# Optimization experiments

Hardware: AMD Instinct MI355X
Metric: run time of the kernel (lower is better)

Reference implementation:

```python
import jax, jax.numpy as jnp
import numpy as np

B, N, CIN, H, OUT, L, K = 8, 512, 64, 64, 64, 256, 3
EPS = 1e-5


def setup_inputs() -> dict:
    key = jax.random.key(0)
    ks = jax.random.split(key, 12)
    def unif(k, shape, fan):
        s = 1.0 / np.sqrt(fan)
        return jax.random.uniform(k, shape, jnp.float32, -s, s)
    return {
        "x": jax.random.normal(ks[0], (B, N, CIN, L), jnp.float32),
        "adj": jax.random.uniform(ks[1], (B, N, N), jnp.float32),
        # temp_conv1: Conv1d(CIN->H, k=3)
        "w1": unif(ks[2], (H, CIN, K), CIN * K),
        "b1": unif(ks[3], (H,), CIN * K),
        # graph_conv: Linear-style (H,H) + bias, stdv=1/sqrt(out_features)
        "gw": unif(ks[4], (H, H), H),
        "gb": unif(ks[5], (H,), H),
        # temp_conv2: Conv1d(H->OUT, k=3)
        "w2": unif(ks[6], (OUT, H, K), H * K),
        "b2": unif(ks[7], (OUT,), H * K),
        # residual: Conv1d(CIN->OUT, k=1) == pointwise linear
        "wr": unif(ks[8], (OUT, CIN), CIN),
        "br": unif(ks[9], (OUT,), CIN),
        # BatchNorm2d(OUT) affine params
        "gamma": jnp.ones((OUT,), jnp.float32),
        "beta": jnp.zeros((OUT,), jnp.float32),
    }


def _conv1d(x, w, b, pad):
    # x: (B, N, C, L) -> flatten node dim into batch, NCH conv
    b_, n_, c, l = x.shape
    y = jax.lax.conv_general_dilated(
        x.reshape(b_ * n_, c, l), w, window_strides=(1,),
        padding=[(pad, pad)], dimension_numbers=("NCH", "OIH", "NCH"))
    y = y + b[None, :, None]
    return y.reshape(b_, n_, w.shape[0], l)


def reference(x, adj, w1, b1, gw, gb, w2, b2, wr, br, gamma, beta):
    pad = (K - 1) // 2
    # residual branch: 1x1 conv over channels
    residual = jnp.einsum("bncl,oc->bnol", x, wr) + br[None, None, :, None]
    # temporal conv 1
    out = _conv1d(x, w1, b1, pad)                      # (B,N,H,L)
    # graph conv over all timesteps at once (replaces per-t Python loop)
    xw = jnp.einsum("bnhl,hd->bndl", out, gw)          # (B,N,H,L)
    out = jnp.einsum("bnm,bmdl->bndl", adj, xw) + gb[None, None, :, None]
    # temporal conv 2
    out = _conv1d(out, w2, b2, pad)                    # (B,N,OUT,L)
    out = out + residual
    # BatchNorm2d over channel axis (training-mode batch stats, biased var)
    mean = jnp.mean(out, axis=(0, 1, 3), keepdims=True)
    var = jnp.mean(jnp.square(out - mean), axis=(0, 1, 3), keepdims=True)
    out = (out - mean) * jax.lax.rsqrt(var + EPS)
    out = out * gamma[None, None, :, None] + beta[None, None, :, None]
    return jax.nn.relu(out)
```

## Files before the change

### kernel.cpp

```cpp
#include <hip/hip_runtime.h>
#include <hip/hip_bf16.h>
#include <stdint.h>


typedef unsigned short u16;
typedef unsigned int   u32;
typedef __attribute__((ext_vector_type(8))) short           bf16x8;
typedef __attribute__((ext_vector_type(8))) unsigned short  u16x8;
typedef __attribute__((ext_vector_type(4))) unsigned short  u16x4;
typedef __attribute__((ext_vector_type(4))) float           f32x4;

__device__ __forceinline__ float bf2f(u16 v){
  union { u32 u; float f; } x; x.u = ((u32)v) << 16; return x.f;
}
__device__ __forceinline__ u16 f2bf(float f){
  __hip_bfloat16 h = __float2bfloat16(f);
  return *reinterpret_cast<u16*>(&h);
}
__device__ __forceinline__ u32 swz(int row, int cbyte){
  return (u32)(row * 128) + (u32)(cbyte ^ ((row & 7) << 4));
}

__device__ __forceinline__ void stage_Tf(const float* __restrict__ src, u16* dst, int t){
  const int c0 = (t & 31) * 2;
  const int l0 = (t >> 5) * 32;
  #pragma unroll
  for (int v = 0; v < 8; ++v){
    f32x4 a = *(const f32x4*)(src + (size_t)c0 * 256 + l0 + v * 4);
    f32x4 b = *(const f32x4*)(src + (size_t)(c0 + 1) * 256 + l0 + v * 4);
    #pragma unroll
    for (int e = 0; e < 4; ++e){
      u32 p = (u32)f2bf(a[e]) | ((u32)f2bf(b[e]) << 16);
      *(u32*)((char*)dst + swz(l0 + v * 4 + e, c0 * 2)) = p;
    }
  }
}
__device__ __forceinline__ void stage_Tb(const u16* __restrict__ src, u16* dst, int t){
  const int c0 = (t & 31) * 2;
  const int l0 = (t >> 5) * 32;
  #pragma unroll
  for (int v = 0; v < 4; ++v){
    u16x8 a = *(const u16x8*)(src + (size_t)c0 * 256 + l0 + v * 8);
    u16x8 b = *(const u16x8*)(src + (size_t)(c0 + 1) * 256 + l0 + v * 8);
    #pragma unroll
    for (int e = 0; e < 8; ++e){
      u32 p = (u32)a[e] | ((u32)b[e] << 16);
      *(u32*)((char*)dst + swz(l0 + v * 8 + e, c0 * 2)) = p;
    }
  }
}

__global__ __launch_bounds__(256) void k_prep(const float* __restrict__ w1, const float* __restrict__ b1,
    const float* __restrict__ gw, const float* __restrict__ w2, const float* __restrict__ wr,
    u16* __restrict__ w1g, float* __restrict__ b1g, u16* __restrict__ w2t, u16* __restrict__ wrt){
  const int gt = blockIdx.x * 256 + threadIdx.x, gs = gridDim.x * 256;
  for (int e = gt; e < 12288; e += gs){
    int tap = e >> 12, rem = e & 4095, o = rem >> 6, c = rem & 63;
    w2t[e] = f2bf(w2[(o * 64 + c) * 3 + tap]);
    float s = 0.f;
    for (int h = 0; h < 64; ++h)
      s += gw[h * 64 + o] * w1[(h * 64 + c) * 3 + tap];
    w1g[e] = f2bf(s);
  }
  for (int e = gt; e < 4096; e += gs) wrt[e] = f2bf(wr[e]);
  for (int d = gt; d < 64; d += gs){
    float s = 0.f;
    for (int h = 0; h < 64; ++h) s += b1[h] * gw[h * 64 + d];
    b1g[d] = s;
  }
}

__global__ __launch_bounds__(256) void k_p1(const float* __restrict__ x,
    const u16* __restrict__ w1g, const float* __restrict__ b1g,
    const u16* __restrict__ wrt, u16* __restrict__ outA, u16* __restrict__ outR){
  __shared__ u16 tile[16384];
  const int t = threadIdx.x;
  const size_t bn = (size_t)blockIdx.x + (size_t)blockIdx.y * 512;
  stage_Tf(x + bn * 16384, tile, t);
  __syncthreads();
  const int w = t >> 6, ln = t & 63, lq = ln >> 4, lr = ln & 15;
  const bf16x8 z8 = {};

  {
    f32x4 racc[4][4];
    #pragma unroll
    for (int i = 0; i < 4; ++i)
      #pragma unroll
      for (int j = 0; j < 4; ++j) racc[i][j] = (f32x4){0.f, 0.f, 0.f, 0.f};
    #pragma unroll
    for (int kk = 0; kk < 2; ++kk){
      bf16x8 A[4];
      #pragma unroll
      for (int fo = 0; fo < 4; ++fo)
        A[fo] = *(const bf16x8*)(wrt + (fo * 16 + lr) * 64 + kk * 32 + lq * 8);
      #pragma unroll
      for (int fc = 0; fc < 4; ++fc){
        int l = w * 64 + fc * 16 + lr;
        bf16x8 B = *(const bf16x8*)((char*)tile + swz(l, kk * 64 + lq * 16));
        #pragma unroll
        for (int fo = 0; fo < 4; ++fo)
          racc[fo][fc] = __builtin_amdgcn_mfma_f32_16x16x32_bf16(A[fo], B, racc[fo][fc], 0, 0, 0);
      }
    }
    u16* rp = outR + bn * 16384 + t * 64;
    #pragma unroll
    for (int v = 0; v < 8; ++v){
      u16x8 ov;
      const int fo = v >> 1;
      #pragma unroll
      for (int h = 0; h < 2; ++h){
        const int fc = (v & 1) * 2 + h;
        #pragma unroll
        for (int r2 = 0; r2 < 4; ++r2)
          ov[h * 4 + r2] = f2bf(racc[fo][fc][r2]);
      }
      *(u16x8*)(rp + v * 8) = ov;
    }
  }

  f32x4 acc[4][4];
  #pragma unroll
  for (int i = 0; i < 4; ++i)
    #pragma unroll
    for (int j = 0; j < 4; ++j) acc[i][j] = (f32x4){0.f, 0.f, 0.f, 0.f};
  #pragma unroll
  for (int tap = 0; tap < 3; ++tap){
    #pragma unroll
    for (int kk = 0; kk < 2; ++kk){
      bf16x8 A[4];
      #pragma unroll
      for (int fo = 0; fo < 4; ++fo)
        A[fo] = *(const bf16x8*)(w1g + tap * 4096 + (fo * 16 + lr) * 64 + kk * 32 + lq * 8);
      #pragma unroll
      for (int fc = 0; fc < 4; ++fc){
        int r = w * 64 + fc * 16 + lr + tap - 1;
        int rc = r < 0 ? 0 : (r > 255 ? 255 : r);
        bf16x8 B = *(const bf16x8*)((char*)tile + swz(rc, kk * 64 + lq * 16));
        if (r != rc) B = z8;
        #pragma unroll
        for (int fo = 0; fo < 4; ++fo)
          acc[fo][fc] = __builtin_amdgcn_mfma_f32_16x16x32_bf16(A[fo], B, acc[fo][fc], 0, 0, 0);
      }
    }
  }
  u16* op = outA + bn * 16384;
  #pragma unroll
  for (int fo = 0; fo < 4; ++fo){
    float bb[4];
    #pragma unroll
    for (int r2 = 0; r2 < 4; ++r2) bb[r2] = b1g[fo * 16 + lq * 4 + r2];
    #pragma unroll
    for (int fc = 0; fc < 4; ++fc){
      int l = w * 64 + fc * 16 + lr;
      #pragma unroll
      for (int r2 = 0; r2 < 4; ++r2)
        op[(fo * 16 + lq * 4 + r2) * 256 + l] = f2bf(acc[fo][fc][r2] + bb[r2]);
    }
  }
}

__global__ __launch_bounds__(256) void k_p3(const u16* __restrict__ xw,
    const float* __restrict__ adj, const float* __restrict__ gbv, u16* __restrict__ outB){
  __shared__ u16 At[8192];
  __shared__ u16 Bt[8192];
  const int t = threadIdx.x;
  const int wg = ((blockIdx.x & 7) << 9) | ((int)blockIdx.x >> 3);
  const int jt = wg & 127, nt = (wg >> 7) & 3, b = wg >> 9;
  const float* adjb = adj + ((size_t)b * 512 + (size_t)nt * 128) * 512;
  const u16* Xb = xw + (size_t)b * 8388608 + (size_t)jt * 128;
  const int w = t >> 6, ln = t & 63, lq = ln >> 4, lr = ln & 15;
  const int wrow = w >> 1, wcol = w & 1;
  const int mpair = t & 31, jq = t >> 5;
  f32x4 acc[4][4];
  #pragma unroll
  for (int i = 0; i < 4; ++i)
    #pragma unroll
    for (int j = 0; j < 4; ++j) acc[i][j] = (f32x4){0.f, 0.f, 0.f, 0.f};

  f32x4 ra[8];
  u16x8 rb[4];
  auto LOADK = [&](int ks){
    #pragma unroll
    for (int it = 0; it < 8; ++it){
      int c = it * 256 + t;
      int row = c >> 4, mc = c & 15;
      ra[it] = *(const f32x4*)(adjb + (size_t)row * 512 + ks * 64 + mc * 4);
    }
    const u16* s0 = Xb + (size_t)(ks * 64 + mpair * 2) * 16384 + jq * 16;
    const u16* s1 = s0 + 16384;
    #pragma unroll
    for (int v2 = 0; v2 < 2; ++v2){
      rb[v2 * 2]     = *(const u16x8*)(s0 + v2 * 8);
      rb[v2 * 2 + 1] = *(const u16x8*)(s1 + v2 * 8);
    }
  };

  LOADK(0);
  for (int ks = 0; ks < 8; ++ks){
    #pragma unroll
    for (int it = 0; it < 8; ++it){
      int c = it * 256 + t;
      int row = c >> 4, mc = c & 15;
      u16x4 pk;
      #pragma unroll
      for (int e = 0; e < 4; ++e) pk[e] = f2bf(ra[it][e]);
      *(u16x4*)((char*)At + (u32)(row * 128) + (u32)((mc * 8) ^ ((row & 7) << 4))) = pk;
    }
    #pragma unroll
    for (int v2 = 0; v2 < 2; ++v2){
      #pragma unroll
      for (int e = 0; e < 8; ++e){
        u32 p = (u32)(u16)rb[v2 * 2][e] | ((u32)(u16)rb[v2 * 2 + 1][e] << 16);
        *(u32*)((char*)Bt + swz(jq * 16 + v2 * 8 + e, mpair * 4)) = p;
      }
    }
    __syncthreads();
    if (ks < 7) LOADK(ks + 1);
    #pragma unroll
    for (int kk = 0; kk < 2; ++kk){
      bf16x8 Af[4], Bf[4];
      #pragma unroll
      for (int f = 0; f < 4; ++f){
        int rA = wrow * 64 + f * 16 + lr;
        Af[f] = *(const bf16x8*)((char*)At + swz(rA, kk * 64 + lq * 16));
        int rB = wcol * 64 + f * 16 + lr;
        Bf[f] = *(const bf16x8*)((char*)Bt + swz(rB, kk * 64 + lq * 16));
      }
      #pragma unroll
      for (int fr = 0; fr < 4; ++fr)
        #pragma unroll
        for (int fc = 0; fc < 4; ++fc)
          acc[fr][fc] = __builtin_amdgcn_mfma_f32_16x16x32_bf16(Af[fr], Bf[fc], acc[fr][fc], 0, 0, 0);
    }
    __syncthreads();
  }
  const float gb = gbv[jt >> 1];
  u16* ob = outB + ((size_t)b * 512 + (size_t)nt * 128) * 16384 + (size_t)jt * 128;
  #pragma unroll
  for (int fr = 0; fr < 4; ++fr)
    #pragma unroll
    for (int fc = 0; fc < 4; ++fc)
      #pragma unroll
      for (int r2 = 0; r2 < 4; ++r2){
        int n_ = wrow * 64 + fr * 16 + lq * 4 + r2;
        int j_ = wcol * 64 + fc * 16 + lr;
        ob[(size_t)n_ * 16384 + j_] = f2bf(acc[fr][fc][r2] + gb);
      }
}

__global__ __launch_bounds__(256) void k_p4(const u16* __restrict__ g,
    const u16* __restrict__ resv, const u16* __restrict__ w2t,
    const float* __restrict__ b2v, const float* __restrict__ brv,
    u16* __restrict__ outP, float* __restrict__ spart){
  __shared__ u16 gt[16384];
  const int t = threadIdx.x;
  const size_t bn = (size_t)blockIdx.x + (size_t)blockIdx.y * 512;
  stage_Tb(g + bn * 16384, gt, t);
  __syncthreads();
  const int w = t >> 6, ln = t & 63, lq = ln >> 4, lr = ln & 15;
  const bf16x8 z8 = {};
  f32x4 acc[4][4];
  #pragma unroll
  for (int i = 0; i < 4; ++i)
    #pragma unroll
    for (int j = 0; j < 4; ++j) acc[i][j] = (f32x4){0.f, 0.f, 0.f, 0.f};

  #pragma unroll
  for (int tap = 0; tap < 3; ++tap){
    #pragma unroll
    for (int kk = 0; kk < 2; ++kk){
      bf16x8 A[4];
      #pragma unroll
      for (int fo = 0; fo < 4; ++fo)
        A[fo] = *(const bf16x8*)(w2t + tap * 4096 + (fo * 16 + lr) * 64 + kk * 32 + lq * 8);
      #pragma unroll
      for (int fc = 0; fc < 4; ++fc){
        int r = w * 64 + fc * 16 + lr + tap - 1;
        int rc = r < 0 ? 0 : (r > 255 ? 255 : r);
        bf16x8 B = *(const bf16x8*)((char*)gt + swz(rc, kk * 64 + lq * 16));
        if (r != rc) B = z8;
        #pragma unroll
        for (int fo = 0; fo < 4; ++fo)
          acc[fo][fc] = __builtin_amdgcn_mfma_f32_16x16x32_bf16(A[fo], B, acc[fo][fc], 0, 0, 0);
      }
    }
  }

  float bball[16];
  #pragma unroll
  for (int fo = 0; fo < 4; ++fo)
    #pragma unroll
    for (int r2 = 0; r2 < 4; ++r2){
      int o = fo * 16 + lq * 4 + r2;
      bball[fo * 4 + r2] = b2v[o] + brv[o];
    }
  float psum[16], psq[16];
  #pragma unroll
  for (int i = 0; i < 16; ++i){ psum[i] = 0.f; psq[i] = 0.f; }

  const u16* rp = resv + bn * 16384 + t * 64;
  u16x8 rv[8];
  #pragma unroll
  for (int v = 0; v < 8; ++v) rv[v] = *(const u16x8*)(rp + v * 8);

  u16* op = outP + bn * 16384;
  #pragma unroll
  for (int fo = 0; fo < 4; ++fo){
    #pragma unroll
    for (int fc = 0; fc < 4; ++fc){
      int l = w * 64 + fc * 16 + lr;
      #pragma unroll
      for (int r2 = 0; r2 < 4; ++r2){
        float val = acc[fo][fc][r2] + bball[fo * 4 + r2]
                  + bf2f(rv[fo * 2 + (fc >> 1)][(fc & 1) * 4 + r2]);
        op[(fo * 16 + lq * 4 + r2) * 256 + l] = f2bf(val);
        psum[fo * 4 + r2] += val;
        psq[fo * 4 + r2] += val * val;
      }
    }
  }

  #pragma unroll
  for (int i = 0; i < 16; ++i){
    #pragma unroll
    for (int m = 1; m < 16; m <<= 1){
      psum[i] += __shfl_xor(psum[i], m, 64);
      psq[i]  += __shfl_xor(psq[i],  m, 64);
    }
  }
  __syncthreads();
  float* sc = (float*)gt;
  if (lr == 0){
    #pragma unroll
    for (int i = 0; i < 16; ++i){
      int o = (i >> 2) * 16 + lq * 4 + (i & 3);
      sc[w * 128 + o]      = psum[i];
      sc[w * 128 + 64 + o] = psq[i];
    }
  }
  __syncthreads();
  if (t < 128){
    float tot = sc[t] + sc[128 + t] + sc[256 + t] + sc[384 + t];
    spart[(size_t)t * 4096 + bn] = tot;
  }
}

__global__ __launch_bounds__(256) void k_p5(const float* __restrict__ part, float* __restrict__ fin){
  const int o = blockIdx.x, t = threadIdx.x;
  float s1 = 0.f, s2 = 0.f;
  for (int k = t; k < 4096; k += 256){
    s1 += part[(size_t)o * 4096 + k];
    s2 += part[(size_t)(64 + o) * 4096 + k];
  }
  #pragma unroll
  for (int m = 32; m; m >>= 1){
    s1 += __shfl_down(s1, m, 64);
    s2 += __shfl_down(s2, m, 64);
  }
  __shared__ float red[8];
  if ((t & 63) == 0){ red[(t >> 6) * 2] = s1; red[(t >> 6) * 2 + 1] = s2; }
  __syncthreads();
  if (t == 0){
    float S1 = red[0] + red[2] + red[4] + red[6];
    float S2 = red[1] + red[3] + red[5] + red[7];
    const float invN = 1.f / 1048576.f;
    float mean = S1 * invN;
    float var = S2 * invN - mean * mean;
    fin[o] = mean;
    fin[64 + o] = rsqrtf(var + 1e-5f);
  }
}

__global__ __launch_bounds__(256) void k_p6(const u16* __restrict__ pre, const float* __restrict__ fin,
    const float* __restrict__ gamma, const float* __restrict__ beta, float* __restrict__ out){
  __shared__ float ssca[64], soff[64];
  const int tt = threadIdx.x;
  if (tt < 64){
    float sc = fin[64 + tt] * gamma[tt];
    ssca[tt] = sc;
    soff[tt] = beta[tt] - fin[tt] * sc;
  }
  __syncthreads();
  const size_t nchunk = 8388608;
  for (size_t i = (size_t)blockIdx.x * 256 + tt; i < nchunk; i += (size_t)gridDim.x * 256){
    int o = (int)((i >> 5) & 63);
    float sca = ssca[o], off = soff[o];
    u16x8 v = *(const u16x8*)(pre + i * 8);
    f32x4 oa, ob;
    #pragma unroll
    for (int e = 0; e < 4; ++e){
      float f0 = bf2f(v[e]) * sca + off;
      float f1 = bf2f(v[4 + e]) * sca + off;
      oa[e] = f0 > 0.f ? f0 : 0.f;
      ob[e] = f1 > 0.f ? f1 : 0.f;
    }
    *(f32x4*)(out + i * 8)     = oa;
    *(f32x4*)(out + i * 8 + 4) = ob;
  }
}

extern "C" void kernel_launch(void* const* d_in, const int* in_sizes, int n_in,
                              void* d_out, int out_size, void* d_ws, size_t ws_size,
                              hipStream_t stream){
  const float* x     = (const float*)d_in[0];
  const float* adj   = (const float*)d_in[1];
  const float* w1    = (const float*)d_in[2];
  const float* b1    = (const float*)d_in[3];
  const float* gw    = (const float*)d_in[4];
  const float* gb    = (const float*)d_in[5];
  const float* w2    = (const float*)d_in[6];
  const float* b2    = (const float*)d_in[7];
  const float* wr    = (const float*)d_in[8];
  const float* br    = (const float*)d_in[9];
  const float* gamma = (const float*)d_in[10];
  const float* beta  = (const float*)d_in[11];
  (void)in_sizes; (void)n_in; (void)out_size; (void)ws_size;

  char* ws = (char*)d_ws;
  u16*   bufA  = (u16*)ws;
  float* spart = (float*)(ws + 134217728);
  float* sfin  = (float*)(ws + 136314880);
  u16*   w1g   = (u16*)(ws + 136315392);
  float* b1g   = (float*)(ws + 136339968);
  u16*   w2t   = (u16*)(ws + 136348160);
  u16*   wrt   = (u16*)(ws + 136372736);
  u16*   gbuf  = (u16*)d_out;
  u16*   bufR  = (u16*)d_out + 67108864;

  k_prep<<<16, 256, 0, stream>>>(w1, b1, gw, w2, wr, w1g, b1g, w2t, wrt);
  k_p1<<<dim3(512, 8, 1), 256, 0, stream>>>(x, w1g, b1g, wrt, bufA, bufR);
  k_p3<<<4096, 256, 0, stream>>>(bufA, adj, gb, gbuf);
  k_p4<<<dim3(512, 8, 1), 256, 0, stream>>>(gbuf, bufR, w2t, b2, br, bufA, spart);
  k_p5<<<64, 256, 0, stream>>>(spart, sfin);
  k_p6<<<2048, 256, 0, stream>>>(bufA, sfin, gamma, beta, (float*)d_out);
}
```

Before: 573.1 us.

## Drop block barriers after LDS staging by making conv reads wave-local

In the first and second temporal-conv kernels, the __syncthreads after staging the input tile into LDS is removed. Each wave now clamps its LDS reads to the 64 rows it staged itself. The halo rows just outside that range are read directly from global memory, converting to bf16 in the first kernel, with zero padding kept at the sequence ends. The residual loads in the second kernel are also issued before the MMA loop so their latency overlaps compute. This removes block-wide synchronisation but adds strided scalar global loads for boundary lanes, and it is correct only if the staging routine assigns each wave exactly its own rows.

Measured after the change: 603.2 us. 1.05x slower.

```diff
diff --git a/kernel.cpp b/kernel.cpp
--- a/kernel.cpp
+++ b/kernel.cpp
@@ -76,9 +76,10 @@
   __shared__ u16 tile[16384];
   const int t = threadIdx.x;
   const size_t bn = (size_t)blockIdx.x + (size_t)blockIdx.y * 512;
-  stage_Tf(x + bn * 16384, tile, t);
-  __syncthreads();
+  const float* xb = x + bn * 16384;
+  stage_Tf(xb, tile, t);
   const int w = t >> 6, ln = t & 63, lq = ln >> 4, lr = ln & 15;
+  const int lo = w * 64, hi = w * 64 + 63;
   const bf16x8 z8 = {};
 
   {
@@ -127,6 +128,7 @@
   for (int tap = 0; tap < 3; ++tap){
     #pragma unroll
     for (int kk = 0; kk < 2; ++kk){
+      const int ch0 = kk * 32 + lq * 8;
       bf16x8 A[4];
       #pragma unroll
       for (int fo = 0; fo < 4; ++fo)
@@ -134,9 +136,18 @@
       #pragma unroll
       for (int fc = 0; fc < 4; ++fc){
         int r = w * 64 + fc * 16 + lr + tap - 1;
-        int rc = r < 0 ? 0 : (r > 255 ? 255 : r);
+        int rc = r < lo ? lo : (r > hi ? hi : r);
         bf16x8 B = *(const bf16x8*)((char*)tile + swz(rc, kk * 64 + lq * 16));
-        if (r != rc) B = z8;
+        if (r != rc){
+          if (r < 0 || r > 255) B = z8;
+          else {
+            bf16x8 f;
+            #pragma unroll
+            for (int e = 0; e < 8; ++e)
+              f[e] = (short)f2bf(xb[(ch0 + e) * 256 + r]);
+            B = f;
+          }
+        }
         #pragma unroll
         for (int fo = 0; fo < 4; ++fo)
           acc[fo][fc] = __builtin_amdgcn_mfma_f32_16x16x32_bf16(A[fo], B, acc[fo][fc], 0, 0, 0);
@@ -255,10 +266,17 @@
   __shared__ u16 gt[16384];
   const int t = threadIdx.x;
   const size_t bn = (size_t)blockIdx.x + (size_t)blockIdx.y * 512;
-  stage_Tb(g + bn * 16384, gt, t);
-  __syncthreads();
+  const u16* gb = g + bn * 16384;
+  stage_Tb(gb, gt, t);
   const int w = t >> 6, ln = t & 63, lq = ln >> 4, lr = ln & 15;
+  const int lo = w * 64, hi = w * 64 + 63;
   const bf16x8 z8 = {};
+
+  const u16* rp = resv + bn * 16384 + t * 64;
+  u16x8 rv[8];
+  #pragma unroll
+  for (int v = 0; v < 8; ++v) rv[v] = *(const u16x8*)(rp + v * 8);
+
   f32x4 acc[4][4];
   #pragma unroll
   for (int i = 0; i < 4; ++i)
@@ -269,6 +287,7 @@
   for (int tap = 0; tap < 3; ++tap){
     #pragma unroll
     for (int kk = 0; kk < 2; ++kk){
+      const int ch0 = kk * 32 + lq * 8;
       bf16x8 A[4];
       #pragma unroll
       for (int fo = 0; fo < 4; ++fo)
@@ -276,9 +295,18 @@
       #pragma unroll
       for (int fc = 0; fc < 4; ++fc){
         int r = w * 64 + fc * 16 + lr + tap - 1;
-        int rc = r < 0 ? 0 : (r > 255 ? 255 : r);
+        int rc = r < lo ? lo : (r > hi ? hi : r);
         bf16x8 B = *(const bf16x8*)((char*)gt + swz(rc, kk * 64 + lq * 16));
-        if (r != rc) B = z8;
+        if (r != rc){
+          if (r < 0 || r > 255) B = z8;
+          else {
+            bf16x8 f;
+            #pragma unroll
+            for (int e = 0; e < 8; ++e)
+              f[e] = (short)gb[(ch0 + e) * 256 + r];
+            B = f;
+          }
+        }
         #pragma unroll
         for (int fo = 0; fo < 4; ++fo)
           acc[fo][fc] = __builtin_amdgcn_mfma_f32_16x16x32_bf16(A[fo], B, acc[fo][fc], 0, 0, 0);
@@ -297,11 +325,6 @@
   float psum[16], psq[16];
   #pragma unroll
   for (int i = 0; i < 16; ++i){ psum[i] = 0.f; psq[i] = 0.f; }
-
-  const u16* rp = resv + bn * 16384 + t * 64;
-  u16x8 rv[8];
-  #pragma unroll
-  for (int v = 0; v < 8; ++v) rv[v] = *(const u16x8*)(rp + v * 8);
 
   u16* op = outP + bn * 16384;
   #pragma unroll
```

## Split output channels into two halves in conv kernels to raise occupancy

Applied to the files above, without the earlier changes.

In k_p1 and k_p4, each wave now computes its output channels in two passes of 32 channels, which halves the live accumulator arrays. The kernels gain launch bounds requesting four blocks per SM, and sched_barrier calls stop the compiler from merging the two passes. k_p4 writes its statistics to a separate shared buffer, removing one __syncthreads that previously guarded reuse of the tile. The cost is that B fragments are reloaded from LDS for each half, and the residual loads and shuffle reductions are split per half.

Measured after the change: 584.2 us. No clear change (+1.9%).

```diff
diff --git a/kernel.cpp b/kernel.cpp
--- a/kernel.cpp
+++ b/kernel.cpp
@@ -70,92 +70,99 @@
   }
 }
 
-__global__ __launch_bounds__(256) void k_p1(const float* __restrict__ x,
+__global__ __launch_bounds__(256, 4) void k_p1(const float* __restrict__ x,
     const u16* __restrict__ w1g, const float* __restrict__ b1g,
     const u16* __restrict__ wrt, u16* __restrict__ outA, u16* __restrict__ outR){
   __shared__ u16 tile[16384];
   const int t = threadIdx.x;
   const size_t bn = (size_t)blockIdx.x + (size_t)blockIdx.y * 512;
-  stage_Tf(x + bn * 16384, tile, t);
+  const float* xb = x + bn * 16384;
+  stage_Tf(xb, tile, t);
   __syncthreads();
   const int w = t >> 6, ln = t & 63, lq = ln >> 4, lr = ln & 15;
   const bf16x8 z8 = {};
 
-  {
-    f32x4 racc[4][4];
-    #pragma unroll
-    for (int i = 0; i < 4; ++i)
+  #pragma unroll
+  for (int h0 = 0; h0 < 2; ++h0){
+    f32x4 racc[2][4];
+    #pragma unroll
+    for (int i = 0; i < 2; ++i)
       #pragma unroll
       for (int j = 0; j < 4; ++j) racc[i][j] = (f32x4){0.f, 0.f, 0.f, 0.f};
     #pragma unroll
     for (int kk = 0; kk < 2; ++kk){
-      bf16x8 A[4];
-      #pragma unroll
-      for (int fo = 0; fo < 4; ++fo)
-        A[fo] = *(const bf16x8*)(wrt + (fo * 16 + lr) * 64 + kk * 32 + lq * 8);
+      bf16x8 A[2];
+      #pragma unroll
+      for (int fi = 0; fi < 2; ++fi)
+        A[fi] = *(const bf16x8*)(wrt + ((h0 * 2 + fi) * 16 + lr) * 64 + kk * 32 + lq * 8);
       #pragma unroll
       for (int fc = 0; fc < 4; ++fc){
         int l = w * 64 + fc * 16 + lr;
         bf16x8 B = *(const bf16x8*)((char*)tile + swz(l, kk * 64 + lq * 16));
         #pragma unroll
-        for (int fo = 0; fo < 4; ++fo)
-          racc[fo][fc] = __builtin_amdgcn_mfma_f32_16x16x32_bf16(A[fo], B, racc[fo][fc], 0, 0, 0);
-      }
-    }
-    u16* rp = outR + bn * 16384 + t * 64;
-    #pragma unroll
-    for (int v = 0; v < 8; ++v){
+        for (int fi = 0; fi < 2; ++fi)
+          racc[fi][fc] = __builtin_amdgcn_mfma_f32_16x16x32_bf16(A[fi], B, racc[fi][fc], 0, 0, 0);
+      }
+    }
+    u16* rp = outR + bn * 16384 + t * 64 + h0 * 32;
+    #pragma unroll
+    for (int v2 = 0; v2 < 4; ++v2){
       u16x8 ov;
-      const int fo = v >> 1;
-      #pragma unroll
-      for (int h = 0; h < 2; ++h){
-        const int fc = (v & 1) * 2 + h;
+      const int fi = v2 >> 1;
+      #pragma unroll
+      for (int hh = 0; hh < 2; ++hh){
+        const int fc = (v2 & 1) * 2 + hh;
         #pragma unroll
         for (int r2 = 0; r2 < 4; ++r2)
-          ov[h * 4 + r2] = f2bf(racc[fo][fc][r2]);
-      }
-      *(u16x8*)(rp + v * 8) = ov;
-    }
-  }
-
-  f32x4 acc[4][4];
-  #pragma unroll
-  for (int i = 0; i < 4; ++i)
-    #pragma unroll
-    for (int j = 0; j < 4; ++j) acc[i][j] = (f32x4){0.f, 0.f, 0.f, 0.f};
-  #pragma unroll
-  for (int tap = 0; tap < 3; ++tap){
-    #pragma unroll
-    for (int kk = 0; kk < 2; ++kk){
-      bf16x8 A[4];
-      #pragma unroll
-      for (int fo = 0; fo < 4; ++fo)
-        A[fo] = *(const bf16x8*)(w1g + tap * 4096 + (fo * 16 + lr) * 64 + kk * 32 + lq * 8);
+          ov[hh * 4 + r2] = f2bf(racc[fi][fc][r2]);
+      }
+      *(u16x8*)(rp + v2 * 8) = ov;
+    }
+    __builtin_amdgcn_sched_barrier(0);
+  }
+
+  u16* op = outA + bn * 16384;
+  #pragma unroll
+  for (int h0 = 0; h0 < 2; ++h0){
+    f32x4 acc[2][4];
+    #pragma unroll
+    for (int i = 0; i < 2; ++i)
+      #pragma unroll
+      for (int j = 0; j < 4; ++j) acc[i][j] = (f32x4){0.f, 0.f, 0.f, 0.f};
+    #pragma unroll
+    for (int tap = 0; tap < 3; ++tap){
+      #pragma unroll
+      for (int kk = 0; kk < 2; ++kk){
+        bf16x8 A[2];
+        #pragma unroll
+        for (int fi = 0; fi < 2; ++fi)
+          A[fi] = *(const bf16x8*)(w1g + tap * 4096 + ((h0 * 2 + fi) * 16 + lr) * 64 + kk * 32 + lq * 8);
+        #pragma unroll
+        for (int fc = 0; fc < 4; ++fc){
+          int r = w * 64 + fc * 16 + lr + tap - 1;
+          int rc = r < 0 ? 0 : (r > 255 ? 255 : r);
+          bf16x8 B = *(const bf16x8*)((char*)tile + swz(rc, kk * 64 + lq * 16));
+          if (r != rc) B = z8;
+          #pragma unroll
+          for (int fi = 0; fi < 2; ++fi)
+            acc[fi][fc] = __builtin_amdgcn_mfma_f32_16x16x32_bf16(A[fi], B, acc[fi][fc], 0, 0, 0);
+        }
+      }
+    }
+    #pragma unroll
+    for (int fi = 0; fi < 2; ++fi){
+      float bb[4];
+      #pragma unroll
+      for (int r2 = 0; r2 < 4; ++r2) bb[r2] = b1g[(h0 * 2 + fi) * 16 + lq * 4 + r2];
       #pragma unroll
       for (int fc = 0; fc < 4; ++fc){
-        int r = w * 64 + fc * 16 + lr + tap - 1;
-        int rc = r < 0 ? 0 : (r > 255 ? 255 : r);
-        bf16x8 B = *(const bf16x8*)((char*)tile + swz(rc, kk * 64 + lq * 16));
-        if (r != rc) B = z8;
-        #pragma unroll
-        for (int fo = 0; fo < 4; ++fo)
-          acc[fo][fc] = __builtin_amdgcn_mfma_f32_16x16x32_bf16(A[fo], B, acc[fo][fc], 0, 0, 0);
-      }
-    }
-  }
-  u16* op = outA + bn * 16384;
-  #pragma unroll
-  for (int fo = 0; fo < 4; ++fo){
-    float bb[4];
-    #pragma unroll
-    for (int r2 = 0; r2 < 4; ++r2) bb[r2] = b1g[fo * 16 + lq * 4 + r2];
-    #pragma unroll
-    for (int fc = 0; fc < 4; ++fc){
-      int l = w * 64 + fc * 16 + lr;
-      #pragma unroll
-      for (int r2 = 0; r2 < 4; ++r2)
-        op[(fo * 16 + lq * 4 + r2) * 256 + l] = f2bf(acc[fo][fc][r2] + bb[r2]);
-    }
+        int l = w * 64 + fc * 16 + lr;
+        #pragma unroll
+        for (int r2 = 0; r2 < 4; ++r2)
+          op[((h0 * 2 + fi) * 16 + lq * 4 + r2) * 256 + l] = f2bf(acc[fi][fc][r2] + bb[r2]);
+      }
+    }
+    __builtin_amdgcn_sched_barrier(0);
   }
 }
 
@@ -248,99 +255,100 @@
       }
 }
 
-__global__ __launch_bounds__(256) void k_p4(const u16* __restrict__ g,
+__global__ __launch_bounds__(256, 4) void k_p4(const u16* __restrict__ g,
     const u16* __restrict__ resv, const u16* __restrict__ w2t,
     const float* __restrict__ b2v, const float* __restrict__ brv,
     u16* __restrict__ outP, float* __restrict__ spart){
   __shared__ u16 gt[16384];
+  __shared__ float sc2[512];
   const int t = threadIdx.x;
   const size_t bn = (size_t)blockIdx.x + (size_t)blockIdx.y * 512;
   stage_Tb(g + bn * 16384, gt, t);
   __syncthreads();
   const int w = t >> 6, ln = t & 63, lq = ln >> 4, lr = ln & 15;
   const bf16x8 z8 = {};
-  f32x4 acc[4][4];
-  #pragma unroll
-  for (int i = 0; i < 4; ++i)
-    #pragma unroll
-    for (int j = 0; j < 4; ++j) acc[i][j] = (f32x4){0.f, 0.f, 0.f, 0.f};
-
-  #pragma unroll
-  for (int tap = 0; tap < 3; ++tap){
-    #pragma unroll
-    for (int kk = 0; kk < 2; ++kk){
-      bf16x8 A[4];
-      #pragma unroll
-      for (int fo = 0; fo < 4; ++fo)
-        A[fo] = *(const bf16x8*)(w2t + tap * 4096 + (fo * 16 + lr) * 64 + kk * 32 + lq * 8);
+  const u16* rp = resv + bn * 16384 + t * 64;
+  u16* op = outP + bn * 16384;
+
+  #pragma unroll
+  for (int h0 = 0; h0 < 2; ++h0){
+    f32x4 acc[2][4];
+    #pragma unroll
+    for (int i = 0; i < 2; ++i)
+      #pragma unroll
+      for (int j = 0; j < 4; ++j) acc[i][j] = (f32x4){0.f, 0.f, 0.f, 0.f};
+
+    u16x8 rv4[4];
+    #pragma unroll
+    for (int v2 = 0; v2 < 4; ++v2) rv4[v2] = *(const u16x8*)(rp + h0 * 32 + v2 * 8);
+
+    #pragma unroll
+    for (int tap = 0; tap < 3; ++tap){
+      #pragma unroll
+      for (int kk = 0; kk < 2; ++kk){
+        bf16x8 A[2];
+        #pragma unroll
+        for (int fi = 0; fi < 2; ++fi)
+          A[fi] = *(const bf16x8*)(w2t + tap * 4096 + ((h0 * 2 + fi) * 16 + lr) * 64 + kk * 32 + lq * 8);
+        #pragma unroll
+        for (int fc = 0; fc < 4; ++fc){
+          int r = w * 64 + fc * 16 + lr + tap - 1;
+          int rc = r < 0 ? 0 : (r > 255 ? 255 : r);
+          bf16x8 B = *(const bf16x8*)((char*)gt + swz(rc, kk * 64 + lq * 16));
+          if (r != rc) B = z8;
+          #pragma unroll
+          for (int fi = 0; fi < 2; ++fi)
+            acc[fi][fc] = __builtin_amdgcn_mfma_f32_16x16x32_bf16(A[fi], B, acc[fi][fc], 0, 0, 0);
+        }
+      }
+    }
+
+    float psum[8], psq[8];
+    #pragma unroll
+    for (int i = 0; i < 8; ++i){ psum[i] = 0.f; psq[i] = 0.f; }
+    #pragma unroll
+    for (int fi = 0; fi < 2; ++fi){
+      float bb[4];
+      #pragma unroll
+      for (int r2 = 0; r2 < 4; ++r2){
+        int o = (h0 * 2 + fi) * 16 + lq * 4 + r2;
+        bb[r2] = b2v[o] + brv[o];
+      }
       #pragma unroll
       for (int fc = 0; fc < 4; ++fc){
-        int r = w * 64 + fc * 16 + lr + tap - 1;
-        int rc = r < 0 ? 0 : (r > 255 ? 255 : r);
-        bf16x8 B = *(const bf16x8*)((char*)gt + swz(rc, kk * 64 + lq * 16));
-        if (r != rc) B = z8;
-        #pragma unroll
-        for (int fo = 0; fo < 4; ++fo)
-          acc[fo][fc] = __builtin_amdgcn_mfma_f32_16x16x32_bf16(A[fo], B, acc[fo][fc], 0, 0, 0);
-      }
-    }
-  }
-
-  float bball[16];
-  #pragma unroll
-  for (int fo = 0; fo < 4; ++fo)
-    #pragma unroll
-    for (int r2 = 0; r2 < 4; ++r2){
-      int o = fo * 16 + lq * 4 + r2;
-      bball[fo * 4 + r2] = b2v[o] + brv[o];
-    }
-  float psum[16], psq[16];
-  #pragma unroll
-  for (int i = 0; i < 16; ++i){ psum[i] = 0.f; psq[i] = 0.f; }
-
-  const u16* rp = resv + bn * 16384 + t * 64;
-  u16x8 rv[8];
-  #pragma unroll
-  for (int v = 0; v < 8; ++v) rv[v] = *(const u16x8*)(rp + v * 8);
-
-  u16* op = outP + bn * 16384;
-  #pragma unroll
-  for (int fo = 0; fo < 4; ++fo){
-    #pragma unroll
-    for (int fc = 0; fc < 4; ++fc){
-      int l = w * 64 + fc * 16 + lr;
-      #pragma unroll
-      for (int r2 = 0; r2 < 4; ++r2){
-        float val = acc[fo][fc][r2] + bball[fo * 4 + r2]
-                  + bf2f(rv[fo * 2 + (fc >> 1)][(fc & 1) * 4 + r2]);
-        op[(fo * 16 + lq * 4 + r2) * 256 + l] = f2bf(val);
-        psum[fo * 4 + r2] += val;
-        psq[fo * 4 + r2] += val * val;
-      }
-    }
-  }
-
-  #pragma unroll
-  for (int i = 0; i < 16; ++i){
-    #pragma unroll
-    for (int m = 1; m < 16; m <<= 1){
-      psum[i] += __shfl_xor(psum[i], m, 64);
-      psq[i]  += __shfl_xor(psq[i],  m, 64);
-    }
-  }
-  __syncthreads();
-  float* sc = (float*)gt;
-  if (lr == 0){
-    #pragma unroll
-    for (int i = 0; i < 16; ++i){
-      int o = (i >> 2) * 16 + lq * 4 + (i & 3);
-      sc[w * 128 + o]      = psum[i];
-      sc[w * 128 + 64 + o] = psq[i];
-    }
-  }
+        int l = w * 64 + fc * 16 + lr;
+        #pragma unroll
+        for (int r2 = 0; r2 < 4; ++r2){
+          float val = acc[fi][fc][r2] + bb[r2]
+                    + bf2f(rv4[fi * 2 + (fc >> 1)][(fc & 1) * 4 + r2]);
+          op[((h0 * 2 + fi) * 16 + lq * 4 + r2) * 256 + l] = f2bf(val);
+          psum[fi * 4 + r2] += val;
+          psq[fi * 4 + r2] += val * val;
+        }
+      }
+    }
+    #pragma unroll
+    for (int i = 0; i < 8; ++i){
+      #pragma unroll
+      for (int m = 1; m < 16; m <<= 1){
+        psum[i] += __shfl_xor(psum[i], m, 64);
+        psq[i]  += __shfl_xor(psq[i],  m, 64);
+      }
+    }
+    if (lr == 0){
+      #pragma unroll
+      for (int i = 0; i < 8; ++i){
+        int o = (h0 * 2 + (i >> 2)) * 16 + lq * 4 + (i & 3);
+        sc2[w * 128 + o]      = psum[i];
+        sc2[w * 128 + 64 + o] = psq[i];
+      }
+    }
+    __builtin_amdgcn_sched_barrier(0);
+  }
+
   __syncthreads();
   if (t < 128){
-    float tot = sc[t] + sc[128 + t] + sc[256 + t] + sc[384 + t];
+    float tot = sc2[t] + sc2[128 + t] + sc2[256 + t] + sc2[384 + t];
     spart[(size_t)t * 4096 + bn] = tot;
   }
 }
```
